# Kernel optimization log

Measured on AMD Instinct MI355X. Metric: run time of the kernel, lower is better.

## Reference

```python
import jax, jax.numpy as jnp
import numpy as np

N = 50000      # nodes
E = 800000     # edges
HID = 64       # hidden_dim
HEADS = 4
DH = HID // HEADS
PIN = 128      # person_in_dim
DIN = 64       # disease_in_dim
NEXP = 4       # num_experts
K = 2          # topk
L = 2          # n_layers
NEG = 0.2      # gat_neg_slope


def setup_inputs() -> dict:
    key = jax.random.key(0)
    ks = iter(jax.random.split(key, 64))
    nrm = lambda shp, s=0.05: jax.random.normal(next(ks), shp, jnp.float32) * s
    d = {}
    d["features"] = jax.random.normal(next(ks), (N, PIN), jnp.float32)
    d["node_types"] = jax.random.randint(next(ks), (N,), 0, 2)
    d["src"] = jax.random.randint(next(ks), (E,), 0, N)
    d["dst"] = jax.random.randint(next(ks), (E,), 0, N)
    d["W_person"] = nrm((PIN, HID)); d["b_person"] = jnp.zeros((HID,), jnp.float32)
    d["W_disease"] = nrm((DIN, HID)); d["b_disease"] = jnp.zeros((HID,), jnp.float32)
    d["gat_W"] = nrm((L, HID, HID)); d["gat_al"] = nrm((L, HEADS, DH)); d["gat_ar"] = nrm((L, HEADS, DH))
    d["gin_eps"] = jnp.zeros((L,), jnp.float32)
    d["gin_W1"] = nrm((L, HID, HID)); d["gin_b1"] = jnp.zeros((L, HID), jnp.float32)
    d["gin_W2"] = nrm((L, HID, HID)); d["gin_b2"] = jnp.zeros((L, HID), jnp.float32)
    for p in ("gat", "gin"):
        d[p + "_gW"] = nrm((HID, NEXP)); d[p + "_gb"] = jnp.zeros((NEXP,), jnp.float32)
        d[p + "_eW1"] = nrm((NEXP, HID, HID // 2)); d[p + "_eb1"] = jnp.zeros((NEXP, HID // 2), jnp.float32)
        d[p + "_eW2"] = nrm((NEXP, HID // 2, HID)); d[p + "_eb2"] = jnp.zeros((NEXP, HID), jnp.float32)
    d["fg_W1"] = nrm((2 * HID, HID)); d["fg_b1"] = jnp.zeros((HID,), jnp.float32)
    d["fg_W2"] = nrm((HID, HID)); d["fg_b2"] = jnp.zeros((HID,), jnp.float32)
    return d


def _edge_softmax(logits, dst):
    m = jax.ops.segment_max(logits, dst, num_segments=N)
    e = jnp.exp(logits - m[dst])
    s = jax.ops.segment_sum(e, dst, num_segments=N)
    return e / (s[dst] + 1e-9)


def _gat(h, src, dst, gat_W, gat_al, gat_ar):
    for l in range(L):
        hW = (h @ gat_W[l]).reshape(N, HEADS, DH)
        el = (hW * gat_al[l]).sum(-1)                    # [N, HEADS]
        er = (hW * gat_ar[l]).sum(-1)
        lg = jax.nn.leaky_relu(el[src] + er[dst], NEG)   # [E, HEADS]
        a = _edge_softmax(lg, dst)
        out = jax.ops.segment_sum(hW[src] * a[:, :, None], dst, num_segments=N)
        h2 = out.reshape(N, HID) + h                     # residual=True
        h = jax.nn.relu(h2) if l < L - 1 else h2
    return h


def _gin(h, src, dst, gin_eps, gin_W1, gin_b1, gin_W2, gin_b2):
    deg = jax.ops.segment_sum(jnp.ones((E,), jnp.float32), dst, num_segments=N)
    inv = 1.0 / jnp.maximum(deg, 1.0)
    for l in range(L):
        agg = jax.ops.segment_sum(h[src], dst, num_segments=N) * inv[:, None]  # 'mean' aggregator
        x = (1.0 + gin_eps[l]) * h + agg                 # learn_eps=True
        x = jax.nn.relu(x @ gin_W1[l] + gin_b1[l]) @ gin_W2[l] + gin_b2[l]     # 2-layer MLP
        h = jax.nn.relu(x) if l < L - 1 else x
    return h


def _expert(h, gW, gb, eW1, eb1, eW2, eb2):
    probs = jax.nn.softmax(h @ gW + gb, axis=-1)         # [N, NEXP]
    topv, topi = jax.lax.top_k(probs, K)
    topv = topv / topv.sum(-1, keepdims=True)
    hot = jax.nn.one_hot(topi, NEXP, dtype=h.dtype)      # [N, K, NEXP]
    w = (hot * topv[..., None]).sum(1)                   # [N, NEXP] sparse weights
    e1 = jax.nn.relu(jnp.einsum('nd,edh->neh', h, eW1) + eb1)
    e2 = jnp.einsum('neh,ehd->ned', e1, eW2) + eb2       # [N, NEXP, HID]
    out = (e2 * w[:, :, None]).sum(1)
    f = hot.sum(1).mean(0)                               # routed fraction per expert
    P = probs.mean(0)
    aux = NEXP * jnp.sum(f * P)                          # switch-style load balancing
    return out, aux


def reference(features, node_types, src, dst, W_person, b_person, W_disease, b_disease,
              gat_W, gat_al, gat_ar, gin_eps, gin_W1, gin_b1, gin_W2, gin_b2,
              gat_gW, gat_gb, gat_eW1, gat_eb1, gat_eW2, gat_eb2,
              gin_gW, gin_gb, gin_eW1, gin_eb1, gin_eW2, gin_eb2,
              fg_W1, fg_b1, fg_W2, fg_b2):
    # per-type projection + scatter into shared buffer
    hp = features[:, :PIN] @ W_person + b_person
    hd = features[:, :DIN] @ W_disease + b_disease
    h = jnp.where((node_types == 0)[:, None], hp, hd)
    z_gat = _gat(h, src, dst, gat_W, gat_al, gat_ar)
    z_gin = _gin(h, src, dst, gin_eps, gin_W1, gin_b1, gin_W2, gin_b2)
    zg, aux_g = _expert(z_gat, gat_gW, gat_gb, gat_eW1, gat_eb1, gat_eW2, gat_eb2)
    zi, aux_i = _expert(z_gin, gin_gW, gin_gb, gin_eW1, gin_eb1, gin_eW2, gin_eb2)
    z = zi * zg
    u = jnp.concatenate([zg, zi], axis=-1)
    gate = jax.nn.sigmoid(jax.nn.relu(u @ fg_W1 + fg_b1) @ fg_W2 + fg_b2)
    u_prime = gate  # source calls fusion_gate(u) twice -> identical deterministic value
    z = gate * z + (1.0 - gate) * u_prime
    return z, aux_i + aux_g
```

## Files before the change

### kernel.cpp

```cpp
#include <hip/hip_runtime.h>

#define NN 50000
#define EE 800000
#define NEG 0.2f
#define NBG 391
#define NBE 196
#define NBKT 98
#define EPB 4096
#define NSEG 196

typedef __attribute__((ext_vector_type(8))) short s8;
typedef __attribute__((ext_vector_type(4))) float f4;

__device__ __forceinline__ float leaky(float x) { return x > 0.f ? x : NEG * x; }
__device__ __forceinline__ unsigned bf16r(float x) {
    unsigned u = __float_as_uint(x);
    return (u + 0x7fffu + ((u >> 16) & 1u)) >> 16;
}
__device__ __forceinline__ float lo16(unsigned p) { return __uint_as_float(p << 16); }
__device__ __forceinline__ float hi16(unsigned p) { return __uint_as_float(p & 0xffff0000u); }

__device__ __forceinline__ s8 a_from_f32(const float* p) {
    float4 u = *reinterpret_cast<const float4*>(p);
    float4 v = *reinterpret_cast<const float4*>(p + 4);
    s8 r;
    r[0] = (short)bf16r(u.x); r[1] = (short)bf16r(u.y);
    r[2] = (short)bf16r(u.z); r[3] = (short)bf16r(u.w);
    r[4] = (short)bf16r(v.x); r[5] = (short)bf16r(v.y);
    r[6] = (short)bf16r(v.z); r[7] = (short)bf16r(v.w);
    return r;
}

__global__ __launch_bounds__(256) void k_binA(const int* __restrict__ src,
        const int* __restrict__ dst,
        int* __restrict__ seg_off, int* __restrict__ seg_cnt,
        unsigned* __restrict__ gseg, int* __restrict__ bucket_tot) {
    __shared__ int cnt[NBKT];
    __shared__ int pre[128];
    __shared__ unsigned sbuf[EPB];
    for (int i = threadIdx.x; i < NBKT; i += 256) cnt[i] = 0;
    __syncthreads();
    int e0 = blockIdx.x * EPB;
    int nE = EE - e0; if (nE > EPB) nE = EPB;
    int b[16]; unsigned val[16]; int rk[16];
    #pragma unroll
    for (int i = 0; i < 16; i++) {
        int li = i * 256 + threadIdx.x;
        if (li < nE) {
            int e = e0 + li;
            int d = dst[e], s = src[e];
            b[i] = d >> 9;
            val[i] = ((unsigned)s << 9) | (unsigned)(d & 511);
            rk[i] = atomicAdd(&cnt[b[i]], 1);
        } else b[i] = -1;
    }
    __syncthreads();
    if (threadIdx.x < 128) pre[threadIdx.x] = (threadIdx.x < NBKT) ? cnt[threadIdx.x] : 0;
    __syncthreads();
    for (int off = 1; off < 128; off <<= 1) {
        int v = 0;
        if (threadIdx.x < 128 && threadIdx.x >= off) v = pre[threadIdx.x - off];
        __syncthreads();
        if (threadIdx.x < 128) pre[threadIdx.x] += v;
        __syncthreads();
    }
    #pragma unroll
    for (int i = 0; i < 16; i++)
        if (b[i] >= 0) sbuf[pre[b[i]] - cnt[b[i]] + rk[i]] = val[i];
    if (threadIdx.x < NBKT) {
        seg_off[blockIdx.x * NBKT + threadIdx.x] = pre[threadIdx.x] - cnt[threadIdx.x];
        seg_cnt[blockIdx.x * NBKT + threadIdx.x] = cnt[threadIdx.x];
        atomicAdd(&bucket_tot[threadIdx.x], cnt[threadIdx.x]);
    }
    __syncthreads();
    for (int i = threadIdx.x; i < nE; i += 256)
        gseg[(size_t)blockIdx.x * EPB + i] = sbuf[i];
}

__global__ __launch_bounds__(256) void k_binB_pre(
        int* __restrict__ row_start, const int* __restrict__ seg_off,
        const int* __restrict__ seg_cnt, const unsigned* __restrict__ gseg,
        int* __restrict__ csr_src, const int* __restrict__ bucket_tot,
        const float* __restrict__ feat, const int* __restrict__ types,
        const float* __restrict__ Wp, const float* __restrict__ bp,
        const float* __restrict__ Wd, const float* __restrict__ bd,
        const float* __restrict__ gW, const float* __restrict__ al,
        const float* __restrict__ ar,
        float* __restrict__ h0f, unsigned* __restrict__ P,
        float* __restrict__ el, float* __restrict__ er) {
    __shared__ unsigned short WpT[64 * 136];
    __shared__ unsigned short WdT[64 * 72];
    __shared__ unsigned short WgT[64 * 72];
    __shared__ unsigned short y0s[4][16 * 72];
    __shared__ int kur[512];
    if (blockIdx.x < NBKT) {
        int b = blockIdx.x;
        int t = threadIdx.x;
        int* spre = (int*)WpT;
        int* soff = (int*)WdT;
        int* ss   = (int*)WgT;
        int* sred = (int*)y0s;
        int bt = (t < b) ? bucket_tot[t] : 0;
        #pragma unroll
        for (int o = 1; o < 64; o <<= 1) bt += __shfl_xor(bt, o, 64);
        if ((t & 63) == 0) sred[t >> 6] = bt;
        int c0 = (2 * t     < NSEG) ? seg_cnt[(2 * t)     * NBKT + b] : 0;
        int c1 = (2 * t + 1 < NSEG) ? seg_cnt[(2 * t + 1) * NBKT + b] : 0;
        if (2 * t     < NSEG) soff[2 * t]     = seg_off[(2 * t)     * NBKT + b];
        if (2 * t + 1 < NSEG) soff[2 * t + 1] = seg_off[(2 * t + 1) * NBKT + b];
        ss[t] = c0 + c1;
        __syncthreads();
        int bstart = sred[0] + sred[1] + sred[2] + sred[3];
        for (int off = 1; off < 256; off <<= 1) {
            int u = (t >= off) ? ss[t - off] : 0;
            __syncthreads();
            ss[t] += u;
            __syncthreads();
        }
        int base = ss[t] - (c0 + c1);
        if (2 * t     < NSEG) spre[2 * t]     = base;
        if (2 * t + 1 < NSEG) spre[2 * t + 1] = base + c0;
        if (t == 0) spre[NSEG] = ss[255];
        for (int i = t; i < 512; i += 256) kur[i] = 0;
        __syncthreads();
        int cntb = spre[NSEG];
        for (int idx = t; idx < cntb; idx += 256) {
            int lo = 0, hi = NSEG - 1;
            #pragma unroll
            for (int s = 0; s < 8; s++) {
                int mid = (lo + hi + 1) >> 1;
                if (spre[mid] <= idx) lo = mid; else hi = mid - 1;
            }
            unsigned v = gseg[(size_t)lo * EPB + soff[lo] + (idx - spre[lo])];
            atomicAdd(&kur[v & 511], 1);
        }
        __syncthreads();
        int s0 = kur[2 * t], s1 = kur[2 * t + 1];
        int pair = s0 + s1;
        ss[t] = pair;
        __syncthreads();
        for (int off = 1; off < 256; off <<= 1) {
            int u = (t >= off) ? ss[t - off] : 0;
            __syncthreads();
            ss[t] += u;
            __syncthreads();
        }
        int epre = ss[t] - pair;
        int cu0 = bstart + epre, cu1 = cu0 + s0;
        kur[2 * t] = cu0; kur[2 * t + 1] = cu1;
        int d0 = b << 9;
        int d = d0 + 2 * t;
        if (d < NN)     row_start[d]     = cu0;
        if (d + 1 < NN) row_start[d + 1] = cu1;
        if (b == 0 && t == 0) row_start[NN] = EE;
        __syncthreads();
        for (int idx = t; idx < cntb; idx += 256) {
            int lo = 0, hi = NSEG - 1;
            #pragma unroll
            for (int s = 0; s < 8; s++) {
                int mid = (lo + hi + 1) >> 1;
                if (spre[mid] <= idx) lo = mid; else hi = mid - 1;
            }
            unsigned v = gseg[(size_t)lo * EPB + soff[lo] + (idx - spre[lo])];
            int p = atomicAdd(&kur[v & 511], 1);
            csr_src[p] = (int)(v >> 9);
        }
        return;
    }
    for (int idx = threadIdx.x; idx < 128 * 64; idx += 256) {
        int k = idx >> 6, n = idx & 63;
        WpT[n * 136 + k] = (unsigned short)bf16r(Wp[idx]);
    }
    for (int idx = threadIdx.x; idx < 64 * 64; idx += 256) {
        int k = idx >> 6, n = idx & 63;
        WdT[n * 72 + k] = (unsigned short)bf16r(Wd[idx]);
        WgT[n * 72 + k] = (unsigned short)bf16r(gW[idx]);
    }
    __syncthreads();
    int wv = threadIdx.x >> 6, lane = threadIdx.x & 63;
    int quad = lane >> 4, l16 = lane & 15;
    int gw2 = (blockIdx.x - NBKT) * 4 + wv;
    int mtEnd = gw2 * 2 + 2; if (mtEnd > 3125) mtEnd = 3125;
    for (int mt = gw2 * 2; mt < mtEnd; mt++) {
        int row0 = mt * 16;
        const float* arow = feat + (size_t)(row0 + l16) * 128;
        f4 accp[4], accd[4];
        #pragma unroll
        for (int t = 0; t < 4; t++) { accp[t] = f4{0.f,0.f,0.f,0.f}; accd[t] = f4{0.f,0.f,0.f,0.f}; }
        #pragma unroll
        for (int ks = 0; ks < 4; ks++) {
            s8 a = a_from_f32(arow + ks * 32 + quad * 8);
            #pragma unroll
            for (int t = 0; t < 4; t++) {
                s8 b = *(const s8*)&WpT[(t * 16 + l16) * 136 + ks * 32 + quad * 8];
                accp[t] = __builtin_amdgcn_mfma_f32_16x16x32_bf16(a, b, accp[t], 0, 0, 0);
                if (ks < 2) {
                    s8 bd_ = *(const s8*)&WdT[(t * 16 + l16) * 72 + ks * 32 + quad * 8];
                    accd[t] = __builtin_amdgcn_mfma_f32_16x16x32_bf16(a, bd_, accd[t], 0, 0, 0);
                }
            }
        }
        int ty[4];
        #pragma unroll
        for (int r = 0; r < 4; r++) ty[r] = types[row0 + quad * 4 + r];
        float vv[4][4];
        #pragma unroll
        for (int t = 0; t < 4; t++) {
            int col = t * 16 + l16;
            float bpv = bp[col], bdv = bd[col];
            #pragma unroll
            for (int r = 0; r < 4; r++) {
                float v = ty[r] ? (accd[t][r] + bdv) : (accp[t][r] + bpv);
                vv[t][r] = v;
                h0f[(size_t)(row0 + quad * 4 + r) * 64 + col] = v;
                y0s[wv][(quad * 4 + r) * 72 + col] = (unsigned short)bf16r(v);
            }
        }
        s8 a0 = *(const s8*)&y0s[wv][l16 * 72 + quad * 8];
        s8 a1 = *(const s8*)&y0s[wv][l16 * 72 + 32 + quad * 8];
        f4 hw[4];
        #pragma unroll
        for (int t = 0; t < 4; t++) {
            hw[t] = f4{0.f,0.f,0.f,0.f};
            s8 b0 = *(const s8*)&WgT[(t * 16 + l16) * 72 + quad * 8];
            hw[t] = __builtin_amdgcn_mfma_f32_16x16x32_bf16(a0, b0, hw[t], 0, 0, 0);
            s8 b1_ = *(const s8*)&WgT[(t * 16 + l16) * 72 + 32 + quad * 8];
            hw[t] = __builtin_amdgcn_mfma_f32_16x16x32_bf16(a1, b1_, hw[t], 0, 0, 0);
        }
        #pragma unroll
        for (int t = 0; t < 4; t++) {
            int col = t * 16 + l16;
            float alv = al[col], arv = ar[col];
            #pragma unroll
            for (int r = 0; r < 4; r++) {
                int row = row0 + quad * 4 + r;
                float h = hw[t][r];
                P[(size_t)row * 64 + col] = bf16r(h) | (bf16r(vv[t][r]) << 16);
                float pl = h * alv, pr = h * arv;
                #pragma unroll
                for (int m = 1; m < 16; m <<= 1) {
                    pl += __shfl_xor(pl, m, 64);
                    pr += __shfl_xor(pr, m, 64);
                }
                if (l16 == 0) {
                    el[(size_t)row * 4 + t] = pl;
                    er[(size_t)row * 4 + t] = pr;
                }
            }
        }
    }
}

template <int RELU>
__global__ void k_edges(const int* __restrict__ rows, const int* __restrict__ csr,
                        const unsigned* __restrict__ Pin,
                        const float* __restrict__ el, const float* __restrict__ er,
                        const float* __restrict__ gat_in, const float* __restrict__ gin_in,
                        const float* __restrict__ eps_p,
                        float* __restrict__ vgf, unsigned short* __restrict__ vgb,
                        unsigned short* __restrict__ xb) {
    __shared__ float ews[4][256];
    int wv = threadIdx.x >> 6, lane = threadIdx.x & 63;
    int n = blockIdx.x * 4 + wv;
    int st = rows[n], dg = rows[n + 1] - st;
    int hd = lane >> 4;
    float4 erv = *reinterpret_cast<const float4*>(er + (size_t)n * 4);
    float accg = 0.f, acci = 0.f, ssum = 0.f;
    for (int base = 0; base < dg; base += 64) {
        int rem = dg - base; if (rem > 64) rem = 64;
        int myi = 0;
        if (lane < rem) {
            myi = csr[st + base + lane];
            float4 lv = *reinterpret_cast<const float4*>(el + (size_t)myi * 4);
            float4 ev;
            ev.x = __expf(leaky(lv.x + erv.x));
            ev.y = __expf(leaky(lv.y + erv.y));
            ev.z = __expf(leaky(lv.z + erv.z));
            ev.w = __expf(leaky(lv.w + erv.w));
            *reinterpret_cast<float4*>(&ews[wv][lane * 4]) = ev;
        }
        int j = 0;
        for (; j + 4 <= rem; j += 4) {
            int s0 = __shfl(myi, j, 64),     s1 = __shfl(myi, j + 1, 64);
            int s2 = __shfl(myi, j + 2, 64), s3 = __shfl(myi, j + 3, 64);
            unsigned p0 = Pin[(size_t)s0 * 64 + lane];
            unsigned p1 = Pin[(size_t)s1 * 64 + lane];
            unsigned p2 = Pin[(size_t)s2 * 64 + lane];
            unsigned p3 = Pin[(size_t)s3 * 64 + lane];
            float a0 = ews[wv][(j + 0) * 4 + hd];
            float a1 = ews[wv][(j + 1) * 4 + hd];
            float a2 = ews[wv][(j + 2) * 4 + hd];
            float a3 = ews[wv][(j + 3) * 4 + hd];
            accg += a0 * lo16(p0) + a1 * lo16(p1) + a2 * lo16(p2) + a3 * lo16(p3);
            acci += hi16(p0) + hi16(p1) + hi16(p2) + hi16(p3);
            ssum += a0 + a1 + a2 + a3;
        }
        for (; j < rem; j++) {
            int s0 = __shfl(myi, j, 64);
            unsigned p0 = Pin[(size_t)s0 * 64 + lane];
            float a0 = ews[wv][j * 4 + hd];
            accg += a0 * lo16(p0); acci += hi16(p0); ssum += a0;
        }
    }
    float vg = accg / (ssum + 1e-9f) + gat_in[(size_t)n * 64 + lane];
    if (RELU) vg = fmaxf(vg, 0.f);
    float invd = 1.0f / fmaxf((float)dg, 1.0f);
    float x = (1.0f + eps_p[0]) * gin_in[(size_t)n * 64 + lane] + acci * invd;
    size_t off = (size_t)n * 64 + lane;
    vgf[off] = vg;
    vgb[off] = (unsigned short)bf16r(vg);
    xb[off] = (unsigned short)bf16r(x);
}

template <int L>
__global__ __launch_bounds__(256) void k_mlp(const unsigned short* __restrict__ Gx,
        const unsigned short* __restrict__ Eb,
        const float* __restrict__ W1, const float* __restrict__ b1,
        const float* __restrict__ W2, const float* __restrict__ b2,
        const float* __restrict__ gatW, const float* __restrict__ al,
        const float* __restrict__ ar,
        unsigned short* __restrict__ Fb, float* __restrict__ Cf,
        unsigned* __restrict__ P, float* __restrict__ el, float* __restrict__ er,
        const float* __restrict__ Zg, const float* __restrict__ ggW,
        const float* __restrict__ ggb, const float* __restrict__ igW,
        const float* __restrict__ igb,
        float* __restrict__ wgtg, float* __restrict__ wgti,
        float* __restrict__ stats) {
    __shared__ unsigned short W1T[64 * 72];
    __shared__ unsigned short W2T[64 * 72];
    __shared__ unsigned short WgT[(L == 0) ? 64 * 72 : 64];
    __shared__ unsigned short y1s[4][16 * 72];
    __shared__ float sstat[16];
    if (L == 1 && threadIdx.x < 16) sstat[threadIdx.x] = 0.f;
    for (int idx = threadIdx.x; idx < 64 * 64; idx += 256) {
        int k = idx >> 6, n = idx & 63;
        W1T[n * 72 + k] = (unsigned short)bf16r(W1[idx]);
        W2T[n * 72 + k] = (unsigned short)bf16r(W2[idx]);
        if (L == 0) WgT[n * 72 + k] = (unsigned short)bf16r(gatW[idx]);
    }
    __syncthreads();
    int wv = threadIdx.x >> 6, lane = threadIdx.x & 63;
    int quad = lane >> 4, l16 = lane & 15;
    int gw = blockIdx.x * 4 + wv;
    int mtEnd = gw * 2 + 2; if (mtEnd > 3125) mtEnd = 3125;
    float sp[2][4] = {{0,0,0,0},{0,0,0,0}};
    float sh[2][4] = {{0,0,0,0},{0,0,0,0}};
    for (int mt = gw * 2; mt < mtEnd; mt++) {
        int row0 = mt * 16;
        const unsigned short* arow = Gx + (size_t)(row0 + l16) * 64;
        s8 a0 = *(const s8*)(arow + quad * 8);
        s8 a1 = *(const s8*)(arow + 32 + quad * 8);
        f4 acc1[4];
        #pragma unroll
        for (int t = 0; t < 4; t++) {
            acc1[t] = f4{0.f,0.f,0.f,0.f};
            s8 b0 = *(const s8*)&W1T[(t * 16 + l16) * 72 + quad * 8];
            acc1[t] = __builtin_amdgcn_mfma_f32_16x16x32_bf16(a0, b0, acc1[t], 0, 0, 0);
            s8 b1_ = *(const s8*)&W1T[(t * 16 + l16) * 72 + 32 + quad * 8];
            acc1[t] = __builtin_amdgcn_mfma_f32_16x16x32_bf16(a1, b1_, acc1[t], 0, 0, 0);
        }
        #pragma unroll
        for (int t = 0; t < 4; t++) {
            float b1v = b1[t * 16 + l16];
            #pragma unroll
            for (int r = 0; r < 4; r++) {
                float v = fmaxf(acc1[t][r] + b1v, 0.f);
                y1s[wv][(quad * 4 + r) * 72 + t * 16 + l16] = (unsigned short)bf16r(v);
            }
        }
        s8 c0 = *(const s8*)&y1s[wv][l16 * 72 + quad * 8];
        s8 c1 = *(const s8*)&y1s[wv][l16 * 72 + 32 + quad * 8];
        f4 acc2[4];
        #pragma unroll
        for (int t = 0; t < 4; t++) {
            acc2[t] = f4{0.f,0.f,0.f,0.f};
            s8 b0 = *(const s8*)&W2T[(t * 16 + l16) * 72 + quad * 8];
            acc2[t] = __builtin_amdgcn_mfma_f32_16x16x32_bf16(c0, b0, acc2[t], 0, 0, 0);
            s8 b1_ = *(const s8*)&W2T[(t * 16 + l16) * 72 + 32 + quad * 8];
            acc2[t] = __builtin_amdgcn_mfma_f32_16x16x32_bf16(c1, b1_, acc2[t], 0, 0, 0);
        }
        unsigned short vb[4][4];
        float vout[4][4];
        #pragma unroll
        for (int t = 0; t < 4; t++) {
            int col = t * 16 + l16;
            float b2v = b2[col];
            #pragma unroll
            for (int r = 0; r < 4; r++) {
                float v = acc2[t][r] + b2v;
                if (L == 0) v = fmaxf(v, 0.f);
                size_t off = (size_t)(row0 + quad * 4 + r) * 64 + col;
                unsigned short vb16 = (unsigned short)bf16r(v);
                vb[t][r] = vb16;
                vout[t][r] = v;
                Fb[off] = vb16;
                if (L == 0) Cf[off] = v;
            }
        }
        if (L == 0) {
            const unsigned short* erow = Eb + (size_t)(row0 + l16) * 64;
            s8 e0 = *(const s8*)(erow + quad * 8);
            s8 e1 = *(const s8*)(erow + 32 + quad * 8);
            f4 hw[4];
            #pragma unroll
            for (int t = 0; t < 4; t++) {
                hw[t] = f4{0.f,0.f,0.f,0.f};
                s8 b0 = *(const s8*)&WgT[(t * 16 + l16) * 72 + quad * 8];
                hw[t] = __builtin_amdgcn_mfma_f32_16x16x32_bf16(e0, b0, hw[t], 0, 0, 0);
                s8 b1_ = *(const s8*)&WgT[(t * 16 + l16) * 72 + 32 + quad * 8];
                hw[t] = __builtin_amdgcn_mfma_f32_16x16x32_bf16(e1, b1_, hw[t], 0, 0, 0);
            }
            #pragma unroll
            for (int t = 0; t < 4; t++) {
                int col = t * 16 + l16;
                float alv = al[col], arv = ar[col];
                #pragma unroll
                for (int r = 0; r < 4; r++) {
                    int row = row0 + quad * 4 + r;
                    float h = hw[t][r];
                    P[(size_t)row * 64 + col] = bf16r(h) | ((unsigned)vb[t][r] << 16);
                    float pl = h * alv, pr = h * arv;
                    #pragma unroll
                    for (int m = 1; m < 16; m <<= 1) {
                        pl += __shfl_xor(pl, m, 64);
                        pr += __shfl_xor(pr, m, 64);
                    }
                    if (l16 == 0) {
                        el[(size_t)row * 4 + t] = pl;
                        er[(size_t)row * 4 + t] = pr;
                    }
                }
            }
        } else {
            #pragma unroll
            for (int r = 0; r < 4; r++) {
                int row = row0 + quad * 4 + r;
                float pg[4] = {0,0,0,0}, pi[4] = {0,0,0,0};
                #pragma unroll
                for (int t = 0; t < 4; t++) {
                    int col = t * 16 + l16;
                    float zgv = Zg[(size_t)row * 64 + col];
                    float ziv = vout[t][r];
                    #pragma unroll
                    for (int e = 0; e < 4; e++) {
                        pg[e] += zgv * ggW[col * 4 + e];
                        pi[e] += ziv * igW[col * 4 + e];
                    }
                }
                #pragma unroll
                for (int m = 1; m < 16; m <<= 1) {
                    #pragma unroll
                    for (int e = 0; e < 4; e++) {
                        pg[e] += __shfl_xor(pg[e], m, 64);
                        pi[e] += __shfl_xor(pi[e], m, 64);
                    }
                }
                if (l16 == 0) {
                    #pragma unroll
                    for (int q = 0; q < 2; q++) {
                        float lg0 = (q ? pi[0] + igb[0] : pg[0] + ggb[0]);
                        float lg1 = (q ? pi[1] + igb[1] : pg[1] + ggb[1]);
                        float lg2 = (q ? pi[2] + igb[2] : pg[2] + ggb[2]);
                        float lg3 = (q ? pi[3] + igb[3] : pg[3] + ggb[3]);
                        float mx = fmaxf(fmaxf(lg0, lg1), fmaxf(lg2, lg3));
                        float ex0 = __expf(lg0 - mx), ex1 = __expf(lg1 - mx);
                        float ex2 = __expf(lg2 - mx), ex3 = __expf(lg3 - mx);
                        float inv = 1.0f / (ex0 + ex1 + ex2 + ex3);
                        float pr4[4] = {ex0 * inv, ex1 * inv, ex2 * inv, ex3 * inv};
                        int i1 = 0; float v1 = pr4[0];
                        #pragma unroll
                        for (int t = 1; t < 4; t++) if (pr4[t] > v1) { v1 = pr4[t]; i1 = t; }
                        int i2 = -1; float v2 = -1.f;
                        #pragma unroll
                        for (int t = 0; t < 4; t++) if (t != i1 && pr4[t] > v2) { v2 = pr4[t]; i2 = t; }
                        float wsum = v1 + v2;
                        float wq[4] = {0.f, 0.f, 0.f, 0.f};
                        wq[i1] = v1 / wsum; wq[i2] = v2 / wsum;
                        float* WD = q ? wgti : wgtg;
                        *reinterpret_cast<float4*>(WD + (size_t)row * 4) =
                            float4{wq[0], wq[1], wq[2], wq[3]};
                        #pragma unroll
                        for (int t = 0; t < 4; t++) sp[q][t] += pr4[t];
                        sh[q][i1] += 1.f; sh[q][i2] += 1.f;
                    }
                }
            }
        }
    }
    if (L == 1) {
        __syncthreads();
        if (l16 == 0) {
            #pragma unroll
            for (int q = 0; q < 2; q++)
                #pragma unroll
                for (int e = 0; e < 4; e++) {
                    atomicAdd(&sstat[q * 8 + e], sp[q][e]);
                    atomicAdd(&sstat[q * 8 + 4 + e], sh[q][e]);
                }
        }
        __syncthreads();
        if (threadIdx.x < 16) atomicAdd(&stats[threadIdx.x], sstat[threadIdx.x]);
    }
}

__global__ __launch_bounds__(256) void k_expert(const unsigned short* __restrict__ Eb,
        const unsigned short* __restrict__ Fb,
        const float* __restrict__ g_eW1, const float* __restrict__ g_eb1,
        const float* __restrict__ g_eW2, const float* __restrict__ g_eb2,
        const float* __restrict__ i_eW1, const float* __restrict__ i_eb1,
        const float* __restrict__ i_eW2, const float* __restrict__ i_eb2,
        const float* __restrict__ wgtg, const float* __restrict__ wgti,
        float* __restrict__ moegf, float* __restrict__ moeif,
        unsigned short* __restrict__ ub) {
    __shared__ unsigned short w1t[4 * 32 * 72];
    __shared__ unsigned short w2t[4 * 64 * 40];
    __shared__ unsigned short y1s[4][16 * 40];
    int p = (blockIdx.x >= NBE) ? 1 : 0;
    int bb = blockIdx.x - p * NBE;
    const unsigned short* Ab = p ? Fb : Eb;
    const float* eW1 = p ? i_eW1 : g_eW1;
    const float* eb1 = p ? i_eb1 : g_eb1;
    const float* eW2 = p ? i_eW2 : g_eW2;
    const float* eb2 = p ? i_eb2 : g_eb2;
    const float* wgt = p ? wgti : wgtg;
    float* moef = p ? moeif : moegf;
    int qoff = p ? 64 : 0;
    for (int g = threadIdx.x; g < 8192; g += 256) {
        int e = g >> 11, rem = g & 2047;
        int k = rem >> 5, n = rem & 31;
        w1t[e * 2304 + n * 72 + k] = (unsigned short)bf16r(eW1[g]);
    }
    for (int g = threadIdx.x; g < 8192; g += 256) {
        int e = g >> 11, rem = g & 2047;
        int k = rem >> 6, n = rem & 63;
        w2t[e * 2560 + n * 40 + k] = (unsigned short)bf16r(eW2[g]);
    }
    __syncthreads();
    int wv = threadIdx.x >> 6, lane = threadIdx.x & 63;
    int quad = lane >> 4, l16 = lane & 15;
    int gw = bb * 4 + wv;
    int mtEnd = gw * 4 + 4; if (mtEnd > 3125) mtEnd = 3125;
    for (int mt = gw * 4; mt < mtEnd; mt++) {
        int row0 = mt * 16;
        const unsigned short* arow = Ab + (size_t)(row0 + l16) * 64;
        s8 a0 = *(const s8*)(arow + quad * 8);
        s8 a1 = *(const s8*)(arow + 32 + quad * 8);
        f4 outacc[4];
        #pragma unroll
        for (int t = 0; t < 4; t++) outacc[t] = f4{0.f,0.f,0.f,0.f};
        for (int e = 0; e < 4; e++) {
            f4 acc1[2];
            #pragma unroll
            for (int t = 0; t < 2; t++) {
                acc1[t] = f4{0.f,0.f,0.f,0.f};
                s8 b0 = *(const s8*)&w1t[e * 2304 + (t * 16 + l16) * 72 + quad * 8];
                acc1[t] = __builtin_amdgcn_mfma_f32_16x16x32_bf16(a0, b0, acc1[t], 0, 0, 0);
                s8 b1_ = *(const s8*)&w1t[e * 2304 + (t * 16 + l16) * 72 + 32 + quad * 8];
                acc1[t] = __builtin_amdgcn_mfma_f32_16x16x32_bf16(a1, b1_, acc1[t], 0, 0, 0);
            }
            #pragma unroll
            for (int t = 0; t < 2; t++) {
                float b1v = eb1[e * 32 + t * 16 + l16];
                #pragma unroll
                for (int r = 0; r < 4; r++) {
                    float v = fmaxf(acc1[t][r] + b1v, 0.f);
                    y1s[wv][(quad * 4 + r) * 40 + t * 16 + l16] = (unsigned short)bf16r(v);
                }
            }
            s8 a2 = *(const s8*)&y1s[wv][l16 * 40 + quad * 8];
            f4 acc2[4];
            #pragma unroll
            for (int t = 0; t < 4; t++) {
                acc2[t] = f4{0.f,0.f,0.f,0.f};
                s8 b2_ = *(const s8*)&w2t[e * 2560 + (t * 16 + l16) * 40 + quad * 8];
                acc2[t] = __builtin_amdgcn_mfma_f32_16x16x32_bf16(a2, b2_, acc2[t], 0, 0, 0);
            }
            #pragma unroll
            for (int t = 0; t < 4; t++) {
                float b2v = eb2[e * 64 + t * 16 + l16];
                #pragma unroll
                for (int r = 0; r < 4; r++) {
                    float we = wgt[(size_t)(row0 + quad * 4 + r) * 4 + e];
                    outacc[t][r] += we * (acc2[t][r] + b2v);
                }
            }
        }
        #pragma unroll
        for (int t = 0; t < 4; t++) {
            int col = t * 16 + l16;
            #pragma unroll
            for (int r = 0; r < 4; r++) {
                int row = row0 + quad * 4 + r;
                float v = outacc[t][r];
                moef[(size_t)row * 64 + col] = v;
                ub[(size_t)row * 128 + qoff + col] = (unsigned short)bf16r(v);
            }
        }
    }
}

__global__ __launch_bounds__(256) void k_fusion(const unsigned short* __restrict__ ubuf,
        const float* __restrict__ W1, const float* __restrict__ b1,
        const float* __restrict__ W2, const float* __restrict__ b2,
        const float* __restrict__ moegf, const float* __restrict__ moeif,
        float* __restrict__ out, const float* __restrict__ stats) {
    __shared__ unsigned short W1T[64 * 136];
    __shared__ unsigned short W2T[64 * 72];
    __shared__ unsigned short y1s[4][16 * 72];
    for (int idx = threadIdx.x; idx < 128 * 64; idx += 256) {
        int k = idx >> 6, n = idx & 63;
        W1T[n * 136 + k] = (unsigned short)bf16r(W1[idx]);
    }
    for (int idx = threadIdx.x; idx < 64 * 64; idx += 256) {
        int k = idx >> 6, n = idx & 63;
        W2T[n * 72 + k] = (unsigned short)bf16r(W2[idx]);
    }
    __syncthreads();
    int wv = threadIdx.x >> 6, lane = threadIdx.x & 63;
    int quad = lane >> 4, l16 = lane & 15;
    int gw = blockIdx.x * 4 + wv;
    int mtEnd = gw * 2 + 2; if (mtEnd > 3125) mtEnd = 3125;
    for (int mt = gw * 2; mt < mtEnd; mt++) {
        int row0 = mt * 16;
        const unsigned short* arow = ubuf + (size_t)(row0 + l16) * 128;
        f4 acc1[4];
        #pragma unroll
        for (int t = 0; t < 4; t++) acc1[t] = f4{0.f,0.f,0.f,0.f};
        #pragma unroll
        for (int ks = 0; ks < 4; ks++) {
            s8 a = *(const s8*)(arow + ks * 32 + quad * 8);
            #pragma unroll
            for (int t = 0; t < 4; t++) {
                s8 b = *(const s8*)&W1T[(t * 16 + l16) * 136 + ks * 32 + quad * 8];
                acc1[t] = __builtin_amdgcn_mfma_f32_16x16x32_bf16(a, b, acc1[t], 0, 0, 0);
            }
        }
        #pragma unroll
        for (int t = 0; t < 4; t++) {
            float b1v = b1[t * 16 + l16];
            #pragma unroll
            for (int r = 0; r < 4; r++) {
                float v = fmaxf(acc1[t][r] + b1v, 0.f);
                y1s[wv][(quad * 4 + r) * 72 + t * 16 + l16] = (unsigned short)bf16r(v);
            }
        }
        f4 acc2[4];
        #pragma unroll
        for (int t = 0; t < 4; t++) acc2[t] = f4{0.f,0.f,0.f,0.f};
        #pragma unroll
        for (int ks = 0; ks < 2; ks++) {
            s8 a = *(const s8*)&y1s[wv][l16 * 72 + ks * 32 + quad * 8];
            #pragma unroll
            for (int t = 0; t < 4; t++) {
                s8 b = *(const s8*)&W2T[(t * 16 + l16) * 72 + ks * 32 + quad * 8];
                acc2[t] = __builtin_amdgcn_mfma_f32_16x16x32_bf16(a, b, acc2[t], 0, 0, 0);
            }
        }
        #pragma unroll
        for (int t = 0; t < 4; t++) {
            int col = t * 16 + l16;
            float b2v = b2[col];
            #pragma unroll
            for (int r = 0; r < 4; r++) {
                int row = row0 + quad * 4 + r;
                float g = 1.0f / (1.0f + __expf(-(acc2[t][r] + b2v)));
                float zgv = moegf[(size_t)row * 64 + col];
                float ziv = moeif[(size_t)row * 64 + col];
                out[(size_t)row * 64 + col] = g * zgv * ziv + (1.0f - g) * g;
            }
        }
    }
    if (blockIdx.x == 0 && threadIdx.x < 64) {
        int t = threadIdx.x;
        float s = (t < 16) ? stats[t] : 0.f;
        float aux = 0.f;
        for (int q = 0; q < 2; q++) {
            float a = 0.f;
            for (int e = 0; e < 4; e++) {
                float pr = __shfl(s, q * 8 + e, 64);
                float f  = __shfl(s, q * 8 + 4 + e, 64);
                a += (f / (float)NN) * (pr / (float)NN);
            }
            aux += 4.0f * a;
        }
        if (t == 0) out[(size_t)NN * 64] = aux;
    }
}

extern "C" void kernel_launch(void* const* d_in, const int* in_sizes, int n_in,
                              void* d_out, int out_size, void* d_ws, size_t ws_size,
                              hipStream_t stream) {
    (void)in_sizes; (void)n_in; (void)out_size; (void)ws_size;
    const float* features  = (const float*)d_in[0];
    const int*   node_types= (const int*)d_in[1];
    const int*   src       = (const int*)d_in[2];
    const int*   dst       = (const int*)d_in[3];
    const float* W_person  = (const float*)d_in[4];
    const float* b_person  = (const float*)d_in[5];
    const float* W_disease = (const float*)d_in[6];
    const float* b_disease = (const float*)d_in[7];
    const float* gat_W     = (const float*)d_in[8];
    const float* gat_al    = (const float*)d_in[9];
    const float* gat_ar    = (const float*)d_in[10];
    const float* gin_eps   = (const float*)d_in[11];
    const float* gin_W1    = (const float*)d_in[12];
    const float* gin_b1    = (const float*)d_in[13];
    const float* gin_W2    = (const float*)d_in[14];
    const float* gin_b2    = (const float*)d_in[15];
    const float* gat_gW    = (const float*)d_in[16];
    const float* gat_gb    = (const float*)d_in[17];
    const float* gat_eW1   = (const float*)d_in[18];
    const float* gat_eb1   = (const float*)d_in[19];
    const float* gat_eW2   = (const float*)d_in[20];
    const float* gat_eb2   = (const float*)d_in[21];
    const float* gin_gW    = (const float*)d_in[22];
    const float* gin_gb    = (const float*)d_in[23];
    const float* gin_eW1   = (const float*)d_in[24];
    const float* gin_eb1   = (const float*)d_in[25];
    const float* gin_eW2   = (const float*)d_in[26];
    const float* gin_eb2   = (const float*)d_in[27];
    const float* fg_W1     = (const float*)d_in[28];
    const float* fg_b1     = (const float*)d_in[29];
    const float* fg_W2     = (const float*)d_in[30];
    const float* fg_b2     = (const float*)d_in[31];
    float* out = (float*)d_out;

    float* ws = (float*)d_ws;
    size_t o = 0;
    float* A = ws + o; o += (size_t)NN * 64;
    float* B = ws + o; o += (size_t)NN * 64;
    float* C = ws + o; o += (size_t)NN * 64;
    unsigned short* E  = (unsigned short*)(ws + o); o += (size_t)NN * 32;
    unsigned short* F  = (unsigned short*)(ws + o); o += (size_t)NN * 32;
    unsigned short* G  = (unsigned short*)(ws + o); o += (size_t)NN * 32;
    unsigned* P = (unsigned*)(ws + o); o += (size_t)NN * 64;
    float* el = ws + o; o += (size_t)NN * 4;
    float* er = ws + o; o += (size_t)NN * 4;
    float* wgtg = ws + o; o += (size_t)NN * 4;
    float* wgti = ws + o; o += (size_t)NN * 4;
    int* bucket_tot = (int*)(ws + o); o += 112;
    float* stats    = ws + o; o += 16;
    int* row_start = (int*)(ws + o); o += NN + 4;
    int* csr_src   = (int*)(ws + o); o += EE;
    int* seg_off   = (int*)(ws + o); o += NSEG * NBKT + 64;
    int* seg_cnt   = (int*)(ws + o); o += NSEG * NBKT + 64;
    unsigned* gseg = (unsigned*)(ws + o); o += (size_t)NSEG * EPB;

    unsigned short* ub = (unsigned short*)A;

    const int NB_node = NN / 4;

    hipMemsetAsync(bucket_tot, 0, sizeof(int) * 112 + sizeof(float) * 16, stream);

    k_binA<<<NSEG, 256, 0, stream>>>(src, dst, seg_off, seg_cnt, gseg, bucket_tot);

    k_binB_pre<<<NBKT + NBG, 256, 0, stream>>>(row_start, seg_off, seg_cnt, gseg, csr_src,
                                               bucket_tot,
                                               features, node_types, W_person, b_person,
                                               W_disease, b_disease, gat_W, gat_al, gat_ar,
                                               A, P, el, er);

    k_edges<1><<<NB_node, 256, 0, stream>>>(row_start, csr_src, P, el, er, A, A,
                                            gin_eps, B, E, G);
    k_mlp<0><<<NBG, 256, 0, stream>>>(G, E, gin_W1, gin_b1, gin_W2, gin_b2,
                                      gat_W + 4096, gat_al + 64, gat_ar + 64,
                                      F, C, P, el, er,
                                      nullptr, nullptr, nullptr, nullptr, nullptr,
                                      nullptr, nullptr, nullptr);

    k_edges<0><<<NB_node, 256, 0, stream>>>(row_start, csr_src, P, el, er, B, C,
                                            gin_eps + 1, B, E, G);
    k_mlp<1><<<NBG, 256, 0, stream>>>(G, nullptr, gin_W1 + 4096, gin_b1 + 64,
                                      gin_W2 + 4096, gin_b2 + 64,
                                      nullptr, nullptr, nullptr,
                                      F, nullptr, nullptr, nullptr, nullptr,
                                      B, gat_gW, gat_gb, gin_gW, gin_gb,
                                      wgtg, wgti, stats);

    k_expert<<<NBE * 2, 256, 0, stream>>>(E, F,
                                          gat_eW1, gat_eb1, gat_eW2, gat_eb2,
                                          gin_eW1, gin_eb1, gin_eW2, gin_eb2,
                                          wgtg, wgti, B, C, ub);

    k_fusion<<<NBG, 256, 0, stream>>>(ub, fg_W1, fg_b1, fg_W2, fg_b2, B, C, out, stats);
}
```

Before: 332.9 us.

## Use finer CSR buckets of 128 nodes to spread CSR build over more blocks

Changes the destination bucketing in the two-pass CSR build from 512-node buckets to 128-node buckets, raising the bucket count from 98 to 391. Each bucket block in the second pass then handles about a quarter of the edges, so more blocks share the scatter work and the critical path per block is shorter. The cost is more per-segment metadata (seg_off/seg_cnt), a larger prefix scan in the first pass, and more global atomics on bucket totals.

```diff
diff --git a/kernel.cpp b/kernel.cpp
--- a/kernel.cpp
+++ b/kernel.cpp
@@ -5,7 +5,7 @@
 #define NEG 0.2f
 #define NBG 391
 #define NBE 196
-#define NBKT 98
+#define NBKT 391
 #define EPB 4096
 #define NSEG 196
 
@@ -35,8 +35,9 @@
         const int* __restrict__ dst,
         int* __restrict__ seg_off, int* __restrict__ seg_cnt,
         unsigned* __restrict__ gseg, int* __restrict__ bucket_tot) {
-    __shared__ int cnt[NBKT];
-    __shared__ int pre[128];
+    __shared__ int cnt[NBKT + 1];
+    __shared__ int pre[512];
+    __shared__ int ssc[256];
     __shared__ unsigned sbuf[EPB];
     for (int i = threadIdx.x; i < NBKT; i += 256) cnt[i] = 0;
     __syncthreads();
@@ -49,31 +50,37 @@
         if (li < nE) {
             int e = e0 + li;
             int d = dst[e], s = src[e];
-            b[i] = d >> 9;
-            val[i] = ((unsigned)s << 9) | (unsigned)(d & 511);
+            b[i] = d >> 7;
+            val[i] = ((unsigned)s << 7) | (unsigned)(d & 127);
             rk[i] = atomicAdd(&cnt[b[i]], 1);
         } else b[i] = -1;
     }
     __syncthreads();
-    if (threadIdx.x < 128) pre[threadIdx.x] = (threadIdx.x < NBKT) ? cnt[threadIdx.x] : 0;
-    __syncthreads();
-    for (int off = 1; off < 128; off <<= 1) {
-        int v = 0;
-        if (threadIdx.x < 128 && threadIdx.x >= off) v = pre[threadIdx.x - off];
-        __syncthreads();
-        if (threadIdx.x < 128) pre[threadIdx.x] += v;
-        __syncthreads();
-    }
+    int t = threadIdx.x;
+    int c0 = (2 * t     < NBKT) ? cnt[2 * t]     : 0;
+    int c1 = (2 * t + 1 < NBKT) ? cnt[2 * t + 1] : 0;
+    ssc[t] = c0 + c1;
+    __syncthreads();
+    for (int off = 1; off < 256; off <<= 1) {
+        int u = (t >= off) ? ssc[t - off] : 0;
+        __syncthreads();
+        ssc[t] += u;
+        __syncthreads();
+    }
+    int base = ssc[t] - (c0 + c1);
+    pre[2 * t] = base;
+    pre[2 * t + 1] = base + c0;
+    __syncthreads();
     #pragma unroll
     for (int i = 0; i < 16; i++)
-        if (b[i] >= 0) sbuf[pre[b[i]] - cnt[b[i]] + rk[i]] = val[i];
-    if (threadIdx.x < NBKT) {
-        seg_off[blockIdx.x * NBKT + threadIdx.x] = pre[threadIdx.x] - cnt[threadIdx.x];
-        seg_cnt[blockIdx.x * NBKT + threadIdx.x] = cnt[threadIdx.x];
-        atomicAdd(&bucket_tot[threadIdx.x], cnt[threadIdx.x]);
-    }
-    __syncthreads();
-    for (int i = threadIdx.x; i < nE; i += 256)
+        if (b[i] >= 0) sbuf[pre[b[i]] + rk[i]] = val[i];
+    for (int i = t; i < NBKT; i += 256) {
+        seg_off[blockIdx.x * NBKT + i] = pre[i];
+        seg_cnt[blockIdx.x * NBKT + i] = cnt[i];
+        atomicAdd(&bucket_tot[i], cnt[i]);
+    }
+    __syncthreads();
+    for (int i = t; i < nE; i += 256)
         gseg[(size_t)blockIdx.x * EPB + i] = sbuf[i];
 }
 
@@ -92,7 +99,7 @@
     __shared__ unsigned short WdT[64 * 72];
     __shared__ unsigned short WgT[64 * 72];
     __shared__ unsigned short y0s[4][16 * 72];
-    __shared__ int kur[512];
+    __shared__ int kur[128];
     if (blockIdx.x < NBKT) {
         int b = blockIdx.x;
         int t = threadIdx.x;
@@ -100,15 +107,14 @@
         int* soff = (int*)WdT;
         int* ss   = (int*)WgT;
         int* sred = (int*)y0s;
-        int bt = (t < b) ? bucket_tot[t] : 0;
-        #pragma unroll
-        for (int o = 1; o < 64; o <<= 1) bt += __shfl_xor(bt, o, 64);
+        int bt = 0;
+        for (int i = t; i < b; i += 256) bt += bucket_tot[i];
+        #pragma unroll
+        for (int o2 = 1; o2 < 64; o2 <<= 1) bt += __shfl_xor(bt, o2, 64);
         if ((t & 63) == 0) sred[t >> 6] = bt;
-        int c0 = (2 * t     < NSEG) ? seg_cnt[(2 * t)     * NBKT + b] : 0;
-        int c1 = (2 * t + 1 < NSEG) ? seg_cnt[(2 * t + 1) * NBKT + b] : 0;
-        if (2 * t     < NSEG) soff[2 * t]     = seg_off[(2 * t)     * NBKT + b];
-        if (2 * t + 1 < NSEG) soff[2 * t + 1] = seg_off[(2 * t + 1) * NBKT + b];
-        ss[t] = c0 + c1;
+        int c0 = (t < NSEG) ? seg_cnt[t * NBKT + b] : 0;
+        if (t < NSEG) soff[t] = seg_off[t * NBKT + b];
+        ss[t] = c0;
         __syncthreads();
         int bstart = sred[0] + sred[1] + sred[2] + sred[3];
         for (int off = 1; off < 256; off <<= 1) {
@@ -117,27 +123,23 @@
             ss[t] += u;
             __syncthreads();
         }
-        int base = ss[t] - (c0 + c1);
-        if (2 * t     < NSEG) spre[2 * t]     = base;
-        if (2 * t + 1 < NSEG) spre[2 * t + 1] = base + c0;
-        if (t == 0) spre[NSEG] = ss[255];
-        for (int i = t; i < 512; i += 256) kur[i] = 0;
-        __syncthreads();
-        int cntb = spre[NSEG];
+        spre[t] = ss[t] - c0;
+        int cntb = ss[255];
+        if (t < 128) kur[t] = 0;
+        __syncthreads();
         for (int idx = t; idx < cntb; idx += 256) {
-            int lo = 0, hi = NSEG - 1;
+            int lo = 0, hi = 255;
             #pragma unroll
             for (int s = 0; s < 8; s++) {
                 int mid = (lo + hi + 1) >> 1;
                 if (spre[mid] <= idx) lo = mid; else hi = mid - 1;
             }
             unsigned v = gseg[(size_t)lo * EPB + soff[lo] + (idx - spre[lo])];
-            atomicAdd(&kur[v & 511], 1);
-        }
-        __syncthreads();
-        int s0 = kur[2 * t], s1 = kur[2 * t + 1];
-        int pair = s0 + s1;
-        ss[t] = pair;
+            atomicAdd(&kur[v & 127], 1);
+        }
+        __syncthreads();
+        int deg = (t < 128) ? kur[t] : 0;
+        ss[t] = deg;
         __syncthreads();
         for (int off = 1; off < 256; off <<= 1) {
             int u = (t >= off) ? ss[t - off] : 0;
@@ -145,25 +147,24 @@
             ss[t] += u;
             __syncthreads();
         }
-        int epre = ss[t] - pair;
-        int cu0 = bstart + epre, cu1 = cu0 + s0;
-        kur[2 * t] = cu0; kur[2 * t + 1] = cu1;
-        int d0 = b << 9;
-        int d = d0 + 2 * t;
-        if (d < NN)     row_start[d]     = cu0;
-        if (d + 1 < NN) row_start[d + 1] = cu1;
+        if (t < 128) {
+            int cur = bstart + ss[t] - deg;
+            kur[t] = cur;
+            int d = (b << 7) + t;
+            if (d < NN) row_start[d] = cur;
+        }
         if (b == 0 && t == 0) row_start[NN] = EE;
         __syncthreads();
         for (int idx = t; idx < cntb; idx += 256) {
-            int lo = 0, hi = NSEG - 1;
+            int lo = 0, hi = 255;
             #pragma unroll
             for (int s = 0; s < 8; s++) {
                 int mid = (lo + hi + 1) >> 1;
                 if (spre[mid] <= idx) lo = mid; else hi = mid - 1;
             }
             unsigned v = gseg[(size_t)lo * EPB + soff[lo] + (idx - spre[lo])];
-            int p = atomicAdd(&kur[v & 511], 1);
-            csr_src[p] = (int)(v >> 9);
+            int p = atomicAdd(&kur[v & 127], 1);
+            csr_src[p] = (int)(v >> 7);
         }
         return;
     }
@@ -738,7 +739,7 @@
     float* er = ws + o; o += (size_t)NN * 4;
     float* wgtg = ws + o; o += (size_t)NN * 4;
     float* wgti = ws + o; o += (size_t)NN * 4;
-    int* bucket_tot = (int*)(ws + o); o += 112;
+    int* bucket_tot = (int*)(ws + o); o += 392;
     float* stats    = ws + o; o += 16;
     int* row_start = (int*)(ws + o); o += NN + 4;
     int* csr_src   = (int*)(ws + o); o += EE;
@@ -750,7 +751,7 @@
 
     const int NB_node = NN / 4;
 
-    hipMemsetAsync(bucket_tot, 0, sizeof(int) * 112 + sizeof(float) * 16, stream);
+    hipMemsetAsync(bucket_tot, 0, sizeof(int) * 392 + sizeof(float) * 16, stream);
 
     k_binA<<<NSEG, 256, 0, stream>>>(src, dst, seg_off, seg_cnt, gseg, bucket_tot);
 
```

Result: faster. 322.5 us (-3.1%).
